# Kernel optimization log

Measured on AMD Instinct MI355X. Metric: run time of the kernel, lower is better.

## Reference

```python
import jax, jax.numpy as jnp
import numpy as np

B, H, S, D = 8, 8, 2048, 64
NEG = -1e9


def setup_inputs() -> dict:
    key = jax.random.key(0)
    k1, k2, k3, k4 = jax.random.split(key, 4)
    query = jax.random.normal(k1, (B, H, S, D), dtype=jnp.float32)
    kk = jax.random.normal(k2, (B, H, S, D), dtype=jnp.float32)
    value = jax.random.normal(k3, (B, H, S, D), dtype=jnp.float32)
    mask = jax.random.randint(k4, (B, S, S), 0, 2, dtype=jnp.int32)
    return {"query": query, "key": kk, "value": value, "mask": mask}


def reference(query, key, value, mask):
    dk = key.shape[-1]
    # scores: [B,H,S,S] = (q/sqrt(dk)) @ k^T
    scores = jnp.einsum('bhqd,bhkd->bhqk', query / np.sqrt(dk), key)
    # mask broadcast over heads: [B,1,S,S]
    scores = jnp.where(mask[:, None, :, :] == 0, NEG, scores)
    attn = jax.nn.softmax(scores.astype(jnp.float32), axis=-1).astype(query.dtype)
    # dropout is identity in eval/deterministic reference
    return jnp.einsum('bhqk,bhkd->bhqd', attn, value)
```

## Files before the change

kernel.cpp:

```cpp
#include <hip/hip_runtime.h>
#include <hip/hip_bf16.h>
#include <stdint.h>


#define B_ 8
#define H_ 8
#define S_ 2048
#define D_ 64
#define QT 128
#define KT 64
#define NT (S_ / KT)
#define TILE_E (KT * D_)
#define LOG2E 1.44269504088896340736f
#define QSCALE (0.125f * LOG2E)

typedef __bf16 bf16;
typedef bf16 bf16x8 __attribute__((ext_vector_type(8)));
typedef float f32x4 __attribute__((ext_vector_type(4)));
typedef unsigned short ushort8_t __attribute__((ext_vector_type(8)));
typedef unsigned long long u64;

#if __has_builtin(__builtin_amdgcn_exp2f)
#define EXP2(x) __builtin_amdgcn_exp2f(x)
#else
#define EXP2(x) exp2f(x)
#endif

static __device__ __forceinline__ unsigned short bfb(float f) {
    bf16 h = (bf16)f;
    return __builtin_bit_cast(unsigned short, h);
}
static __device__ __forceinline__ int phi_inv(int c) {
    return ((c >> 5) & 1) * 32 + ((c >> 2) & 1) * 16 + ((c >> 4) & 1) * 8 +
           ((c >> 3) & 1) * 4 + (c & 3);
}
static __device__ __forceinline__ void gload16(const unsigned short* g, unsigned short* l) {
    __builtin_amdgcn_global_load_lds(
        (const __attribute__((address_space(1))) unsigned int*)g,
        (__attribute__((address_space(3))) unsigned int*)l, 16, 0, 0);
}

#define KV_BLOCKS (B_ * H_ * NT)

__global__ __launch_bounds__(256) void prep_fused(
    const float* __restrict__ K, const float* __restrict__ V,
    unsigned short* __restrict__ Ko, unsigned short* __restrict__ Vo,
    const int* __restrict__ M, u64* __restrict__ W) {
    const int tid = threadIdx.x;
    if (blockIdx.x >= KV_BLOCKS) {
        const int ln = tid & 63;
        const int w0 = (blockIdx.x - KV_BLOCKS) * 32 + (tid >> 6) * 8;
#pragma unroll
        for (int j = 0; j < 8; ++j) {
            const int v = M[(long)(w0 + j) * 64 + ln];
            const u64 bal = __ballot(v != 0);
            if (ln == 0) W[w0 + j] = bal;
        }
        return;
    }
    if (Ko == nullptr) return;
    __shared__ float Vl[64][65];
    const int t = blockIdx.x & (NT - 1);
    const int bh = blockIdx.x >> 5;
    const float* Kg = K + ((long)bh * S_ + t * 64) * D_;
    const float* Vg = V + ((long)bh * S_ + t * 64) * D_;
    unsigned short* Kout = Ko + ((long)bh * S_ + t * 64) * D_;
    unsigned short* Vout = Vo + (long)bh * D_ * S_ + t * 64;
    {
        const int kv = tid >> 2, d0 = (tid & 3) * 16;
#pragma unroll
        for (int half = 0; half < 2; ++half) {
            const float4 f0 = *(const float4*)(Kg + kv * D_ + d0 + half * 8);
            const float4 f1 = *(const float4*)(Kg + kv * D_ + d0 + half * 8 + 4);
            ushort8_t u;
            u[0] = bfb(f0.x); u[1] = bfb(f0.y); u[2] = bfb(f0.z); u[3] = bfb(f0.w);
            u[4] = bfb(f1.x); u[5] = bfb(f1.y); u[6] = bfb(f1.z); u[7] = bfb(f1.w);
            *(ushort8_t*)(Kout + kv * D_ + d0 + half * 8) = u;
        }
    }
    {
#pragma unroll
        for (int i = 0; i < 4; ++i) {
            const int kv = i * 16 + (tid >> 4);
            const int d4 = (tid & 15) * 4;
            const float4 f = *(const float4*)(Vg + kv * D_ + d4);
            Vl[kv][d4 + 0] = f.x; Vl[kv][d4 + 1] = f.y;
            Vl[kv][d4 + 2] = f.z; Vl[kv][d4 + 3] = f.w;
        }
    }
    __syncthreads();
    {
#pragma unroll
        for (int j = 0; j < 4; ++j) {
            const int chunk = j * 256 + tid;
            const int d = chunk >> 4, q4 = chunk & 15;
            ushort4 w;
            w.x = bfb(Vl[phi_inv(q4 * 4 + 0)][d]);
            w.y = bfb(Vl[phi_inv(q4 * 4 + 1)][d]);
            w.z = bfb(Vl[phi_inv(q4 * 4 + 2)][d]);
            w.w = bfb(Vl[phi_inv(q4 * 4 + 3)][d]);
            *(ushort4*)(Vout + (long)d * S_ + q4 * 4) = w;
        }
    }
}

__global__ __launch_bounds__(256, 2) void attn_main(
    const float* __restrict__ Q, const u64* __restrict__ W,
    const unsigned short* __restrict__ Kp, const unsigned short* __restrict__ Vp,
    float* __restrict__ O)
{
    __shared__ __attribute__((aligned(16))) unsigned short Ks3[4 * TILE_E];
    __shared__ __attribute__((aligned(16))) unsigned short Vt3[4 * TILE_E];

    const int tid = threadIdx.x;
    const int wv = tid >> 6, ln = tid & 63;
    const int col = ln & 15, grp = ln >> 4;

    int bid = blockIdx.x;
    bid = (bid & 7) * 128 + (bid >> 3);
    const int qt = bid & 15;
    const int h = (bid >> 4) & 7;
    const int b = bid >> 7;
    const int qa = qt * QT + wv * 32;

    bf16x8 qfa[2], qfb[2];
    {
        const float* Qga = Q + ((long)((b * H_ + h) * S_) + qa + col) * D_;
        const float* Qgb = Qga + 16 * D_;
#pragma unroll
        for (int c = 0; c < 2; ++c) {
            const float4 a0 = *(const float4*)(Qga + c * 32 + grp * 8);
            const float4 a1 = *(const float4*)(Qga + c * 32 + grp * 8 + 4);
            qfa[c][0] = (bf16)(a0.x * QSCALE); qfa[c][1] = (bf16)(a0.y * QSCALE);
            qfa[c][2] = (bf16)(a0.z * QSCALE); qfa[c][3] = (bf16)(a0.w * QSCALE);
            qfa[c][4] = (bf16)(a1.x * QSCALE); qfa[c][5] = (bf16)(a1.y * QSCALE);
            qfa[c][6] = (bf16)(a1.z * QSCALE); qfa[c][7] = (bf16)(a1.w * QSCALE);
            const float4 b0 = *(const float4*)(Qgb + c * 32 + grp * 8);
            const float4 b1 = *(const float4*)(Qgb + c * 32 + grp * 8 + 4);
            qfb[c][0] = (bf16)(b0.x * QSCALE); qfb[c][1] = (bf16)(b0.y * QSCALE);
            qfb[c][2] = (bf16)(b0.z * QSCALE); qfb[c][3] = (bf16)(b0.w * QSCALE);
            qfb[c][4] = (bf16)(b1.x * QSCALE); qfb[c][5] = (bf16)(b1.y * QSCALE);
            qfb[c][6] = (bf16)(b1.z * QSCALE); qfb[c][7] = (bf16)(b1.w * QSCALE);
        }
    }
    bf16x8 onesf;
#pragma unroll
    for (int j = 0; j < 8; ++j) onesf[j] = (bf16)1.0f;

    f32x4 oaccA[4], oaccB[4];
#pragma unroll
    for (int i = 0; i < 4; ++i) {
        oaccA[i] = (f32x4){0.f, 0.f, 0.f, 0.f};
        oaccB[i] = (f32x4){0.f, 0.f, 0.f, 0.f};
    }
    f32x4 accsA = (f32x4){0.f, 0.f, 0.f, 0.f};
    f32x4 accsB = (f32x4){0.f, 0.f, 0.f, 0.f};

    const u64* Wa = W + ((long)b * S_ + qa + col) * (S_ / 64);
    const u64* Wb = Wa + 16 * (S_ / 64);
    const unsigned short* Kbh = Kp + (long)(b * H_ + h) * S_ * D_;
    const unsigned short* Vbh = Vp + (long)(b * H_ + h) * D_ * S_;

    const int rl = ln >> 3;
    const int c8 = (ln & 7) ^ rl;

    auto STAGE_ISSUE = [&](int kv0, int buf) {
#pragma unroll
        for (int i = 0; i < 2; ++i) {
            const int row = i * 32 + wv * 8 + rl;
            gload16(Kbh + (long)(kv0 + row) * D_ + c8 * 8,
                    Ks3 + buf * TILE_E + i * 2048 + wv * 512);
            gload16(Vbh + (long)row * S_ + kv0 + c8 * 8,
                    Vt3 + buf * TILE_E + i * 2048 + wv * 512);
        }
    };

    auto STEP = [&](u64 mwa, u64 mwb, const unsigned short* Kc, const unsigned short* Vc) {
        f32x4 sa[4], sb[4];
        {
            const u64 ma = mwa >> (grp * 4), mb = mwb >> (grp * 4);
            const unsigned alo = (unsigned)ma, ahi = (unsigned)(ma >> 32);
            const unsigned blo = (unsigned)mb, bhi = (unsigned)(mb >> 32);
#pragma unroll
            for (int blk = 0; blk < 4; ++blk) {
                const unsigned wa32 = (blk < 2) ? alo : ahi;
                const unsigned wb32 = (blk < 2) ? blo : bhi;
#pragma unroll
                for (int r = 0; r < 4; ++r) {
                    const int bit = (blk & 1) * 16 + r;
                    sa[blk][r] = ((wa32 >> bit) & 1u) ? 0.0f : -1e9f;
                    sb[blk][r] = ((wb32 >> bit) & 1u) ? 0.0f : -1e9f;
                }
            }
        }
        __builtin_amdgcn_s_setprio(1);
#pragma unroll
        for (int blk = 0; blk < 4; ++blk) {
            const int row = blk * 16 + col;
            const int byte0 = (row * 128 + grp * 16) ^ ((row & 7) << 4);
            const int byte1 = (row * 128 + 64 + grp * 16) ^ ((row & 7) << 4);
            const bf16x8 kf0 = *(const bf16x8*)((const char*)Kc + byte0);
            const bf16x8 kf1 = *(const bf16x8*)((const char*)Kc + byte1);
            sa[blk] = __builtin_amdgcn_mfma_f32_16x16x32_bf16(kf0, qfa[0], sa[blk], 0, 0, 0);
            sa[blk] = __builtin_amdgcn_mfma_f32_16x16x32_bf16(kf1, qfa[1], sa[blk], 0, 0, 0);
            sb[blk] = __builtin_amdgcn_mfma_f32_16x16x32_bf16(kf0, qfb[0], sb[blk], 0, 0, 0);
            sb[blk] = __builtin_amdgcn_mfma_f32_16x16x32_bf16(kf1, qfb[1], sb[blk], 0, 0, 0);
        }
        __builtin_amdgcn_s_setprio(0);
        bf16x8 pa[2], pb[2];
#pragma unroll
        for (int c = 0; c < 2; ++c)
#pragma unroll
            for (int j = 0; j < 8; ++j) {
                const int blk = 2 * c + (j >> 2), r = j & 3;
                pa[c][j] = (bf16)EXP2(sa[blk][r]);
                pb[c][j] = (bf16)EXP2(sb[blk][r]);
            }
        __builtin_amdgcn_s_setprio(1);
        accsA = __builtin_amdgcn_mfma_f32_16x16x32_bf16(pa[0], onesf, accsA, 0, 0, 0);
        accsA = __builtin_amdgcn_mfma_f32_16x16x32_bf16(pa[1], onesf, accsA, 0, 0, 0);
        accsB = __builtin_amdgcn_mfma_f32_16x16x32_bf16(pb[0], onesf, accsB, 0, 0, 0);
        accsB = __builtin_amdgcn_mfma_f32_16x16x32_bf16(pb[1], onesf, accsB, 0, 0, 0);
#pragma unroll
        for (int c = 0; c < 2; ++c)
#pragma unroll
            for (int db = 0; db < 4; ++db) {
                const int vrow = db * 16 + col;
                const int byte = (vrow * 128 + c * 64 + grp * 16) ^ ((vrow & 7) << 4);
                const bf16x8 vf = *(const bf16x8*)((const char*)Vc + byte);
                oaccA[db] = __builtin_amdgcn_mfma_f32_16x16x32_bf16(pa[c], vf, oaccA[db], 0, 0, 0);
                oaccB[db] = __builtin_amdgcn_mfma_f32_16x16x32_bf16(pb[c], vf, oaccB[db], 0, 0, 0);
            }
        __builtin_amdgcn_s_setprio(0);
    };

#define WAIT4_BAR() do { asm volatile("s_waitcnt vmcnt(4)" ::: "memory"); \
    __builtin_amdgcn_s_barrier(); __builtin_amdgcn_sched_barrier(0); } while (0)
#define WAIT0_BAR() do { asm volatile("s_waitcnt vmcnt(0)" ::: "memory"); \
    __builtin_amdgcn_s_barrier(); __builtin_amdgcn_sched_barrier(0); } while (0)

    STAGE_ISSUE(0, 0);
    STAGE_ISSUE(KT, 1);
    WAIT4_BAR();

#pragma unroll 1
    for (int tt = 0; tt < NT - 4; tt += 4) {
#pragma unroll
        for (int j = 0; j < 4; ++j) {
            const int t = tt + j;
            const u64 mwa = Wa[t], mwb = Wb[t];
            STAGE_ISSUE((t + 2) * KT, (j + 2) & 3);
            STEP(mwa, mwb, Ks3 + j * TILE_E, Vt3 + j * TILE_E);
            WAIT4_BAR();
        }
    }
    {
        {
            const u64 mwa = Wa[NT - 4], mwb = Wb[NT - 4];
            STAGE_ISSUE((NT - 2) * KT, (NT - 2) & 3);
            STEP(mwa, mwb, Ks3 + ((NT - 4) & 3) * TILE_E, Vt3 + ((NT - 4) & 3) * TILE_E);
            WAIT4_BAR();
        }
        {
            const u64 mwa = Wa[NT - 3], mwb = Wb[NT - 3];
            STAGE_ISSUE((NT - 1) * KT, (NT - 1) & 3);
            STEP(mwa, mwb, Ks3 + ((NT - 3) & 3) * TILE_E, Vt3 + ((NT - 3) & 3) * TILE_E);
            WAIT4_BAR();
        }
        {
            const u64 mwa = Wa[NT - 2], mwb = Wb[NT - 2];
            STEP(mwa, mwb, Ks3 + ((NT - 2) & 3) * TILE_E, Vt3 + ((NT - 2) & 3) * TILE_E);
            WAIT0_BAR();
        }
        {
            const u64 mwa = Wa[NT - 1], mwb = Wb[NT - 1];
            STEP(mwa, mwb, Ks3 + ((NT - 1) & 3) * TILE_E, Vt3 + ((NT - 1) & 3) * TILE_E);
        }
    }

    float* Oa = O + ((long)((b * H_ + h) * S_) + qa) * D_;
#pragma unroll
    for (int r = 0; r < 4; ++r) {
        const float ia = 1.0f / accsA[r];
        const float ib = 1.0f / accsB[r];
#pragma unroll
        for (int db = 0; db < 4; ++db) {
            Oa[(grp * 4 + r) * D_ + db * 16 + col] = oaccA[db][r] * ia;
            Oa[(16 + grp * 4 + r) * D_ + db * 16 + col] = oaccB[db][r] * ib;
        }
    }
#undef WAIT4_BAR
#undef WAIT0_BAR
}

template <int MODE>
__global__ __launch_bounds__(512, 4) void attn_fb(
    const float* __restrict__ Q, const float* __restrict__ K,
    const float* __restrict__ V, const int* __restrict__ M,
    const u64* __restrict__ W, float* __restrict__ O)
{
    __shared__ __attribute__((aligned(16))) unsigned short Ks2[2 * TILE_E];
    __shared__ __attribute__((aligned(16))) unsigned short Vt2[2 * TILE_E];

    const int tid = threadIdx.x;
    const int wv = tid >> 6, ln = tid & 63;
    const int col = ln & 15, grp = ln >> 4;

    int bid = blockIdx.x;
    bid = (bid & 7) * 128 + (bid >> 3);
    const int qt = bid & 15;
    const int h = (bid >> 4) & 7;
    const int b = bid >> 7;
    const int qw = qt * QT + wv * 16;

    const float* Qg = Q + ((long)((b * H_ + h) * S_) + qw + col) * D_;
    bf16x8 qf[2];
#pragma unroll
    for (int c = 0; c < 2; ++c) {
        const float4 a0 = *(const float4*)(Qg + c * 32 + grp * 8);
        const float4 a1 = *(const float4*)(Qg + c * 32 + grp * 8 + 4);
        qf[c][0] = (bf16)(a0.x * QSCALE); qf[c][1] = (bf16)(a0.y * QSCALE);
        qf[c][2] = (bf16)(a0.z * QSCALE); qf[c][3] = (bf16)(a0.w * QSCALE);
        qf[c][4] = (bf16)(a1.x * QSCALE); qf[c][5] = (bf16)(a1.y * QSCALE);
        qf[c][6] = (bf16)(a1.z * QSCALE); qf[c][7] = (bf16)(a1.w * QSCALE);
    }
    bf16x8 onesf;
#pragma unroll
    for (int j = 0; j < 8; ++j) onesf[j] = (bf16)1.0f;

    f32x4 oacc[4];
#pragma unroll
    for (int i = 0; i < 4; ++i) oacc[i] = (f32x4){0.f, 0.f, 0.f, 0.f};
    f32x4 accs = (f32x4){0.f, 0.f, 0.f, 0.f};

    const u64* Wg = (MODE >= 1) ? (W + ((long)b * S_ + qw + col) * (S_ / 64)) : nullptr;
    const int* Mg = (MODE == 0) ? (M + ((long)b * S_ + qw + col) * S_) : nullptr;
    const float* Kf = K + (long)(b * H_ + h) * S_ * D_;
    const float* Vf = V + (long)(b * H_ + h) * S_ * D_;

    float4 ka[2];
    float va[8];
    const int vd = ln, kg0 = wv;

    auto LOADT = [&](int kv0) {
#pragma unroll
        for (int i = 0; i < 2; ++i) {
            const int idx4 = i * 512 + tid;
            const int row = idx4 >> 4, c4 = idx4 & 15;
            ka[i] = *(const float4*)(Kf + (long)(kv0 + row) * D_ + c4 * 4);
        }
#pragma unroll
        for (int i = 0; i < 2; ++i) {
            const int kg = kg0 + i * 8;
            const int kvn = phi_inv(kg * 4);
#pragma unroll
            for (int j = 0; j < 4; ++j)
                va[i * 4 + j] = Vf[(long)(kv0 + kvn + j) * D_ + vd];
        }
    };
    auto WRITET = [&](int buf) {
#pragma unroll
        for (int i = 0; i < 2; ++i) {
            const int idx4 = i * 512 + tid;
            const int row = idx4 >> 4, c4 = idx4 & 15;
            const int byte = (row * 128 + c4 * 8) ^ ((row & 7) << 4);
            ushort4 w;
            w.x = bfb(ka[i].x); w.y = bfb(ka[i].y);
            w.z = bfb(ka[i].z); w.w = bfb(ka[i].w);
            *(ushort4*)((char*)(Ks2 + buf * TILE_E) + byte) = w;
        }
#pragma unroll
        for (int i = 0; i < 2; ++i) {
            const int kg = kg0 + i * 8;
            const int byte = (vd * 128 + kg * 8) ^ ((vd & 7) << 4);
            ushort4 w;
            w.x = bfb(va[i * 4 + 0]); w.y = bfb(va[i * 4 + 1]);
            w.z = bfb(va[i * 4 + 2]); w.w = bfb(va[i * 4 + 3]);
            *(ushort4*)((char*)(Vt2 + buf * TILE_E) + byte) = w;
        }
    };
    auto FSTEP = [&](u64 mwfull, int t, const unsigned short* Kc, const unsigned short* Vc) {
        f32x4 sc[4];
        const f32x4 zq = (f32x4){0.f, 0.f, 0.f, 0.f};
#pragma unroll
        for (int blk = 0; blk < 4; ++blk) {
            const int row = blk * 16 + col;
            const int byte0 = (row * 128 + grp * 16) ^ ((row & 7) << 4);
            const int byte1 = (row * 128 + 64 + grp * 16) ^ ((row & 7) << 4);
            const bf16x8 kf0 = *(const bf16x8*)((const char*)Kc + byte0);
            const bf16x8 kf1 = *(const bf16x8*)((const char*)Kc + byte1);
            sc[blk] = __builtin_amdgcn_mfma_f32_16x16x32_bf16(kf0, qf[0], zq, 0, 0, 0);
            sc[blk] = __builtin_amdgcn_mfma_f32_16x16x32_bf16(kf1, qf[1], sc[blk], 0, 0, 0);
        }
        bf16x8 pf[2];
        if (MODE >= 1) {
            const u64 mws = mwfull >> (grp * 4);
            const unsigned mlo = (unsigned)mws, mhi = (unsigned)(mws >> 32);
#pragma unroll
            for (int c = 0; c < 2; ++c)
#pragma unroll
                for (int j = 0; j < 8; ++j) {
                    const int blk = 2 * c + (j >> 2), r = j & 3;
                    const unsigned w32 = (blk < 2) ? mlo : mhi;
                    const int bit = (blk & 1) * 16 + r;
                    const float s = ((w32 >> bit) & 1u) ? sc[blk][r] : -1e9f;
                    pf[c][j] = (bf16)EXP2(s);
                }
        } else {
#pragma unroll
            for (int c = 0; c < 2; ++c)
#pragma unroll
                for (int j = 0; j < 8; ++j) {
                    const int blk = 2 * c + (j >> 2), r = j & 3;
                    const int mv = Mg[t * KT + blk * 16 + grp * 4 + r];
                    const float s = mv ? sc[blk][r] : -1e9f;
                    pf[c][j] = (bf16)EXP2(s);
                }
        }
        accs = __builtin_amdgcn_mfma_f32_16x16x32_bf16(pf[0], onesf, accs, 0, 0, 0);
        accs = __builtin_amdgcn_mfma_f32_16x16x32_bf16(pf[1], onesf, accs, 0, 0, 0);
#pragma unroll
        for (int c = 0; c < 2; ++c)
#pragma unroll
            for (int db = 0; db < 4; ++db) {
                const int vrow = db * 16 + col;
                const int byte = (vrow * 128 + c * 64 + grp * 16) ^ ((vrow & 7) << 4);
                const bf16x8 vf = *(const bf16x8*)((const char*)Vc + byte);
                oacc[db] = __builtin_amdgcn_mfma_f32_16x16x32_bf16(pf[c], vf, oacc[db], 0, 0, 0);
            }
    };

    LOADT(0);
    WRITET(0);
    __syncthreads();
#pragma unroll 1
    for (int t = 0; t < NT; t += 2) {
        if (t + 1 < NT) LOADT((t + 1) * KT);
        FSTEP(MODE >= 1 ? Wg[t] : 0ull, t, Ks2, Vt2);
        if (t + 1 < NT) WRITET(1);
        __syncthreads();
        if (t + 2 < NT) LOADT((t + 2) * KT);
        FSTEP(MODE >= 1 ? Wg[t + 1] : 0ull, t + 1, Ks2 + TILE_E, Vt2 + TILE_E);
        if (t + 2 < NT) WRITET(0);
        __syncthreads();
    }

    float* Og = O + ((long)((b * H_ + h) * S_) + qw) * D_;
#pragma unroll
    for (int r = 0; r < 4; ++r) {
        const float inv = 1.0f / accs[r];
#pragma unroll
        for (int db = 0; db < 4; ++db)
            Og[(grp * 4 + r) * D_ + db * 16 + col] = oacc[db][r] * inv;
    }
}

extern "C" void kernel_launch(void* const* d_in, const int* in_sizes, int n_in,
                              void* d_out, int out_size, void* d_ws, size_t ws_size,
                              hipStream_t stream) {
    (void)in_sizes; (void)n_in; (void)out_size;
    const float* Q = (const float*)d_in[0];
    const float* K = (const float*)d_in[1];
    const float* V = (const float*)d_in[2];
    const int*   M = (const int*)d_in[3];
    float* O = (float*)d_out;

    const size_t szW = (size_t)B_ * S_ * (S_ / 64) * sizeof(u64);
    const size_t szK = (size_t)B_ * H_ * S_ * D_ * 2;
    const int grid = B_ * H_ * (S_ / QT);
    const int nmaskblk = (B_ * S_ * (S_ / 64)) / 32;

    if (ws_size >= szW + 2 * szK) {
        u64* W = (u64*)d_ws;
        unsigned short* Kp = (unsigned short*)((char*)d_ws + szW);
        unsigned short* Vp = (unsigned short*)((char*)d_ws + szW + szK);
        prep_fused<<<KV_BLOCKS + nmaskblk, 256, 0, stream>>>(K, V, Kp, Vp, M, W);
        attn_main<<<grid, 256, 0, stream>>>(Q, W, Kp, Vp, O);
    } else if (ws_size >= szW) {
        u64* W = (u64*)d_ws;
        prep_fused<<<KV_BLOCKS + nmaskblk, 256, 0, stream>>>(K, V, nullptr, nullptr, M, W);
        attn_fb<1><<<grid, 512, 0, stream>>>(Q, K, V, M, W, O);
    } else {
        attn_fb<0><<<grid, 512, 0, stream>>>(Q, K, V, M, nullptr, O);
    }
}
```

Measured before the change: 164.8 us.

## Use double-buffered LDS pipeline and scalar row sums with higher occupancy

Replaces the 4-deep LDS ring (prefetch distance 2, vmcnt(4) waits) with a 2-buffer ping-pong that waits for all loads each step. The launch bound now targets 4 blocks per CU instead of 2. The MFMA-with-ones row-sum is replaced by VALU accumulation of exponentials plus cross-lane shuffles at the end. This halves LDS use and removes four MFMAs per step, but it shortens prefetch lookahead, adds VALU adds, and tighter register limits may cause spills.

```diff
diff --git a/kernel.cpp b/kernel.cpp
--- a/kernel.cpp
+++ b/kernel.cpp
@@ -104,13 +104,13 @@
     }
 }
 
-__global__ __launch_bounds__(256, 2) void attn_main(
+__global__ __launch_bounds__(256, 4) void attn_main(
     const float* __restrict__ Q, const u64* __restrict__ W,
     const unsigned short* __restrict__ Kp, const unsigned short* __restrict__ Vp,
     float* __restrict__ O)
 {
-    __shared__ __attribute__((aligned(16))) unsigned short Ks3[4 * TILE_E];
-    __shared__ __attribute__((aligned(16))) unsigned short Vt3[4 * TILE_E];
+    __shared__ __attribute__((aligned(16))) unsigned short Ks2[2 * TILE_E];
+    __shared__ __attribute__((aligned(16))) unsigned short Vt2[2 * TILE_E];
 
     const int tid = threadIdx.x;
     const int wv = tid >> 6, ln = tid & 63;
@@ -143,9 +143,6 @@
             qfb[c][6] = (bf16)(b1.z * QSCALE); qfb[c][7] = (bf16)(b1.w * QSCALE);
         }
     }
-    bf16x8 onesf;
-#pragma unroll
-    for (int j = 0; j < 8; ++j) onesf[j] = (bf16)1.0f;
 
     f32x4 oaccA[4], oaccB[4];
 #pragma unroll
@@ -153,8 +150,7 @@
         oaccA[i] = (f32x4){0.f, 0.f, 0.f, 0.f};
         oaccB[i] = (f32x4){0.f, 0.f, 0.f, 0.f};
     }
-    f32x4 accsA = (f32x4){0.f, 0.f, 0.f, 0.f};
-    f32x4 accsB = (f32x4){0.f, 0.f, 0.f, 0.f};
+    float dsumA = 0.f, dsumB = 0.f;
 
     const u64* Wa = W + ((long)b * S_ + qa + col) * (S_ / 64);
     const u64* Wb = Wa + 16 * (S_ / 64);
@@ -169,9 +165,9 @@
         for (int i = 0; i < 2; ++i) {
             const int row = i * 32 + wv * 8 + rl;
             gload16(Kbh + (long)(kv0 + row) * D_ + c8 * 8,
-                    Ks3 + buf * TILE_E + i * 2048 + wv * 512);
+                    Ks2 + buf * TILE_E + i * 2048 + wv * 512);
             gload16(Vbh + (long)row * S_ + kv0 + c8 * 8,
-                    Vt3 + buf * TILE_E + i * 2048 + wv * 512);
+                    Vt2 + buf * TILE_E + i * 2048 + wv * 512);
         }
     };
 
@@ -213,14 +209,14 @@
 #pragma unroll
             for (int j = 0; j < 8; ++j) {
                 const int blk = 2 * c + (j >> 2), r = j & 3;
-                pa[c][j] = (bf16)EXP2(sa[blk][r]);
-                pb[c][j] = (bf16)EXP2(sb[blk][r]);
+                const float ea = EXP2(sa[blk][r]);
+                const float eb = EXP2(sb[blk][r]);
+                dsumA += ea;
+                dsumB += eb;
+                pa[c][j] = (bf16)ea;
+                pb[c][j] = (bf16)eb;
             }
         __builtin_amdgcn_s_setprio(1);
-        accsA = __builtin_amdgcn_mfma_f32_16x16x32_bf16(pa[0], onesf, accsA, 0, 0, 0);
-        accsA = __builtin_amdgcn_mfma_f32_16x16x32_bf16(pa[1], onesf, accsA, 0, 0, 0);
-        accsB = __builtin_amdgcn_mfma_f32_16x16x32_bf16(pb[0], onesf, accsB, 0, 0, 0);
-        accsB = __builtin_amdgcn_mfma_f32_16x16x32_bf16(pb[1], onesf, accsB, 0, 0, 0);
 #pragma unroll
         for (int c = 0; c < 2; ++c)
 #pragma unroll
@@ -234,62 +230,43 @@
         __builtin_amdgcn_s_setprio(0);
     };
 
-#define WAIT4_BAR() do { asm volatile("s_waitcnt vmcnt(4)" ::: "memory"); \
-    __builtin_amdgcn_s_barrier(); __builtin_amdgcn_sched_barrier(0); } while (0)
 #define WAIT0_BAR() do { asm volatile("s_waitcnt vmcnt(0)" ::: "memory"); \
     __builtin_amdgcn_s_barrier(); __builtin_amdgcn_sched_barrier(0); } while (0)
 
     STAGE_ISSUE(0, 0);
-    STAGE_ISSUE(KT, 1);
-    WAIT4_BAR();
+    WAIT0_BAR();
 
 #pragma unroll 1
-    for (int tt = 0; tt < NT - 4; tt += 4) {
-#pragma unroll
-        for (int j = 0; j < 4; ++j) {
-            const int t = tt + j;
+    for (int t = 0; t < NT; t += 2) {
+        {
             const u64 mwa = Wa[t], mwb = Wb[t];
-            STAGE_ISSUE((t + 2) * KT, (j + 2) & 3);
-            STEP(mwa, mwb, Ks3 + j * TILE_E, Vt3 + j * TILE_E);
-            WAIT4_BAR();
-        }
-    }
-    {
+            if (t + 1 < NT) STAGE_ISSUE((t + 1) * KT, 1);
+            STEP(mwa, mwb, Ks2, Vt2);
+            WAIT0_BAR();
+        }
         {
-            const u64 mwa = Wa[NT - 4], mwb = Wb[NT - 4];
-            STAGE_ISSUE((NT - 2) * KT, (NT - 2) & 3);
-            STEP(mwa, mwb, Ks3 + ((NT - 4) & 3) * TILE_E, Vt3 + ((NT - 4) & 3) * TILE_E);
-            WAIT4_BAR();
-        }
-        {
-            const u64 mwa = Wa[NT - 3], mwb = Wb[NT - 3];
-            STAGE_ISSUE((NT - 1) * KT, (NT - 1) & 3);
-            STEP(mwa, mwb, Ks3 + ((NT - 3) & 3) * TILE_E, Vt3 + ((NT - 3) & 3) * TILE_E);
-            WAIT4_BAR();
-        }
-        {
-            const u64 mwa = Wa[NT - 2], mwb = Wb[NT - 2];
-            STEP(mwa, mwb, Ks3 + ((NT - 2) & 3) * TILE_E, Vt3 + ((NT - 2) & 3) * TILE_E);
+            const u64 mwa = Wa[t + 1], mwb = Wb[t + 1];
+            if (t + 2 < NT) STAGE_ISSUE((t + 2) * KT, 0);
+            STEP(mwa, mwb, Ks2 + TILE_E, Vt2 + TILE_E);
             WAIT0_BAR();
         }
-        {
-            const u64 mwa = Wa[NT - 1], mwb = Wb[NT - 1];
-            STEP(mwa, mwb, Ks3 + ((NT - 1) & 3) * TILE_E, Vt3 + ((NT - 1) & 3) * TILE_E);
-        }
-    }
-
+    }
+
+    dsumA += __shfl_xor(dsumA, 16);
+    dsumA += __shfl_xor(dsumA, 32);
+    dsumB += __shfl_xor(dsumB, 16);
+    dsumB += __shfl_xor(dsumB, 32);
     float* Oa = O + ((long)((b * H_ + h) * S_) + qa) * D_;
 #pragma unroll
     for (int r = 0; r < 4; ++r) {
-        const float ia = 1.0f / accsA[r];
-        const float ib = 1.0f / accsB[r];
+        const float ia = 1.0f / __shfl(dsumA, grp * 20 + r);
+        const float ib = 1.0f / __shfl(dsumB, grp * 20 + r);
 #pragma unroll
         for (int db = 0; db < 4; ++db) {
             Oa[(grp * 4 + r) * D_ + db * 16 + col] = oaccA[db][r] * ia;
             Oa[(16 + grp * 4 + r) * D_ + db * 16 + col] = oaccB[db][r] * ib;
         }
     }
-#undef WAIT4_BAR
 #undef WAIT0_BAR
 }
 
@@ -311,7 +288,7 @@
     const int qt = bid & 15;
     const int h = (bid >> 4) & 7;
     const int b = bid >> 7;
-    const int qw = qt * QT + wv * 16;
+    const int qw = qt * 128 + wv * 16;
 
     const float* Qg = Q + ((long)((b * H_ + h) * S_) + qw + col) * D_;
     bf16x8 qf[2];
@@ -467,7 +444,6 @@
 
     const size_t szW = (size_t)B_ * S_ * (S_ / 64) * sizeof(u64);
     const size_t szK = (size_t)B_ * H_ * S_ * D_ * 2;
-    const int grid = B_ * H_ * (S_ / QT);
     const int nmaskblk = (B_ * S_ * (S_ / 64)) / 32;
 
     if (ws_size >= szW + 2 * szK) {
@@ -475,12 +451,12 @@
         unsigned short* Kp = (unsigned short*)((char*)d_ws + szW);
         unsigned short* Vp = (unsigned short*)((char*)d_ws + szW + szK);
         prep_fused<<<KV_BLOCKS + nmaskblk, 256, 0, stream>>>(K, V, Kp, Vp, M, W);
-        attn_main<<<grid, 256, 0, stream>>>(Q, W, Kp, Vp, O);
+        attn_main<<<B_ * H_ * (S_ / QT), 256, 0, stream>>>(Q, W, Kp, Vp, O);
     } else if (ws_size >= szW) {
         u64* W = (u64*)d_ws;
         prep_fused<<<KV_BLOCKS + nmaskblk, 256, 0, stream>>>(K, V, nullptr, nullptr, M, W);
-        attn_fb<1><<<grid, 512, 0, stream>>>(Q, K, V, M, W, O);
+        attn_fb<1><<<1024, 512, 0, stream>>>(Q, K, V, M, W, O);
     } else {
-        attn_fb<0><<<grid, 512, 0, stream>>>(Q, K, V, M, nullptr, O);
-    }
-}
+        attn_fb<0><<<1024, 512, 0, stream>>>(Q, K, V, M, nullptr, O);
+    }
+}
```

After: 195.6 us. 18.7% more time.
